# Kernel optimization log

Measured on AMD Instinct MI355X. Metric: run time of the kernel, lower is better.

## Reference

```python
import jax, jax.numpy as jnp
import numpy as np

N_MAX_L = (24, 20, 16, 12)   # basis size per angular channel l
N_SPECIES = 4
HIDDEN = 32
N_PAIRS = 1_500_000


def setup_inputs() -> dict:
    key = jax.random.key(0)
    ks = jax.random.split(key, 2 + 4 * len(N_MAX_L))
    inp = {
        "radial_functions": jax.random.normal(ks[0], (N_PAIRS, sum(N_MAX_L)), jnp.float32),
        "neighbor_species": jax.random.randint(ks[1], (N_PAIRS,), 0, N_SPECIES),
    }
    i = 2
    for l, n in enumerate(N_MAX_L):
        inp[f"w1_l{l}"] = jax.random.normal(ks[i], (N_SPECIES, n, HIDDEN), jnp.float32) * (n ** -0.5); i += 1
        inp[f"w2_l{l}"] = jax.random.normal(ks[i], (N_SPECIES, HIDDEN, HIDDEN), jnp.float32) * (HIDDEN ** -0.5); i += 1
        inp[f"w3_l{l}"] = jax.random.normal(ks[i], (N_SPECIES, HIDDEN, HIDDEN), jnp.float32) * (HIDDEN ** -0.5); i += 1
        inp[f"w4_l{l}"] = jax.random.normal(ks[i], (N_SPECIES, HIDDEN, n), jnp.float32) * (HIDDEN ** -0.5); i += 1
    return inp


def _species_mlp(x, neighbor_species, w1, w2, w3, w4):
    # x: [N, n_l]; weights: [S, ...]. For each row, apply the MLP of its species.
    # Equivalent to the torch gather -> tiny MLP -> scatter per species.
    out = jnp.zeros_like(x)
    for s in range(N_SPECIES):
        h = jax.nn.silu(x @ w1[s])
        h = jax.nn.silu(h @ w2[s])
        h = jax.nn.silu(h @ w3[s])
        y = h @ w4[s]
        out = jnp.where((neighbor_species == s)[:, None], y, out)
    return out


def reference(radial_functions, neighbor_species,
              w1_l0, w2_l0, w3_l0, w4_l0,
              w1_l1, w2_l1, w3_l1, w4_l1,
              w1_l2, w2_l2, w3_l2, w4_l2,
              w1_l3, w2_l3, w3_l3, w4_l3):
    ws = [(w1_l0, w2_l0, w3_l0, w4_l0),
          (w1_l1, w2_l1, w3_l1, w4_l1),
          (w1_l2, w2_l2, w3_l2, w4_l2),
          (w1_l3, w2_l3, w3_l3, w4_l3)]
    outs = []
    idx = 0
    for l, n in enumerate(N_MAX_L):
        x = radial_functions[:, idx:idx + n]
        idx += n
        outs.append(_species_mlp(x, neighbor_species, *ws[l]))
    # torch version returns a list of per-l blocks; we return them concatenated
    # along the feature axis ([N, sum(n_max_l)]) for a single-array output.
    return jnp.concatenate(outs, axis=1)
```

## Files before the change

kernel.cpp:

```cpp
#include <hip/hip_runtime.h>

typedef __attribute__((ext_vector_type(8))) short bf16x8;
typedef __attribute__((ext_vector_type(16))) float f32x16;

union FragU { bf16x8 v; unsigned int u[4]; };
struct Wptrs { const float* p[16]; };

#define ROWS 256
#define THREADS 512

__device__ __forceinline__ unsigned int bfb(float f) {
  unsigned int u = __builtin_bit_cast(unsigned int, f);
  return (u + 0x7fffu + ((u >> 16) & 1u)) >> 16;
}
__device__ __forceinline__ unsigned int cvtpk(float lo, float hi) {
  unsigned int d;
  asm("v_cvt_pk_bf16_f32 %0, %1, %2" : "=v"(d) : "v"(lo), "v"(hi));
  return d;
}
__device__ __forceinline__ float bf2f(unsigned short b) {
  return __builtin_bit_cast(float, (unsigned int)b << 16);
}
__device__ __forceinline__ float silu_f(float x) {
  float e = __builtin_amdgcn_exp2f(-1.4426950408889634f * x);
  return x * __builtin_amdgcn_rcpf(1.0f + e);
}
__device__ __forceinline__ f32x16 zero16() {
  f32x16 z;
  #pragma unroll
  for (int i = 0; i < 16; ++i) z[i] = 0.0f;
  return z;
}
__device__ __forceinline__ bf16x8 ldA(const unsigned short* __restrict__ wsb, int tile, int l31, int hi, int h) {
  return *(const bf16x8*)(wsb + ((tile * 32 + l31) << 5) + h * 16 + hi * 8);
}

__device__ __forceinline__ void transition(const f32x16& acc, bf16x8& b0, bf16x8& b1) {
  unsigned int P[8];
  #pragma unroll
  for (int t = 0; t < 8; ++t)
    P[t] = cvtpk(silu_f(acc[2*t]), silu_f(acc[2*t+1]));
  asm volatile("v_permlane32_swap_b32 %0, %1" : "+v"(P[0]), "+v"(P[2]));
  asm volatile("v_permlane32_swap_b32 %0, %1" : "+v"(P[1]), "+v"(P[3]));
  asm volatile("v_permlane32_swap_b32 %0, %1" : "+v"(P[4]), "+v"(P[6]));
  asm volatile("v_permlane32_swap_b32 %0, %1" : "+v"(P[5]), "+v"(P[7]));
  FragU f0, f1;
  f0.u[0] = P[0]; f0.u[1] = P[1]; f0.u[2] = P[2]; f0.u[3] = P[3];
  f1.u[0] = P[4]; f1.u[1] = P[5]; f1.u[2] = P[6]; f1.u[3] = P[7];
  b0 = f0.v; b1 = f1.v;
}

template<int NL, int OFF, int TB, int SI>
__device__ __forceinline__ void phase(const float* __restrict__ rad,
    const unsigned short* __restrict__ wsb,
    unsigned short* s_in, unsigned short* s_out, const unsigned short* s_pos,
    const int* s_cnt, const int* s_off, const int* s_gpre,
    int base, int vb, int tid)
{
  constexpr int QPR = NL / 4;
  __syncthreads();
  {
    int4 z = make_int4(0, 0, 0, 0);
    #pragma unroll
    for (int i = 0; i < (ROWS * 32) / (8 * THREADS); ++i)
      ((int4*)s_in)[i * THREADS + tid] = z;
  }
  __syncthreads();
  for (int j = tid; j < vb * QPR; j += THREADS) {
    int i = j / QPR, q = j - i * QPR;
    float4 g = *(const float4*)(rad + (long)(base + i) * 72 + OFF + q * 4);
    int dst = s_pos[i];
    *(uint2*)(s_in + dst * SI + q * 4) = make_uint2(cvtpk(g.x, g.y), cvtpk(g.z, g.w));
  }
  __syncthreads();

  const int lane = tid & 63, wid = tid >> 6;
  const int l31 = lane & 31, hi = lane >> 5;
  const int Gtot = s_gpre[4];
  for (int g = wid; g < Gtot; g += THREADS / 64) {
    int s = (g >= s_gpre[1]) + (g >= s_gpre[2]) + (g >= s_gpre[3]);
    int gi = g - s_gpre[s];
    int goff = s_off[s] + gi * 32;
    int gcnt = s_cnt[s] - gi * 32; if (gcnt > 32) gcnt = 32;
    int li = l31 < gcnt ? l31 : gcnt - 1;
    int row = goff + li;

    FragU bx0, bx1;
    bx0.v = *(const bf16x8*)(s_in + row * SI + hi * 8);
    if (NL > 16) bx1.v = *(const bf16x8*)(s_in + row * SI + 16 + hi * 8);

    f32x16 acc = zero16();
    acc = __builtin_amdgcn_mfma_f32_32x32x16_bf16(ldA(wsb, TB + s, l31, hi, 0), bx0.v, acc, 0, 0, 0);
    if (NL > 16)
      acc = __builtin_amdgcn_mfma_f32_32x32x16_bf16(ldA(wsb, TB + s, l31, hi, 1), bx1.v, acc, 0, 0, 0);
    bf16x8 b0, b1;
    transition(acc, b0, b1);
    acc = zero16();
    acc = __builtin_amdgcn_mfma_f32_32x32x16_bf16(ldA(wsb, TB + 4 + s, l31, hi, 0), b0, acc, 0, 0, 0);
    acc = __builtin_amdgcn_mfma_f32_32x32x16_bf16(ldA(wsb, TB + 4 + s, l31, hi, 1), b1, acc, 0, 0, 0);
    transition(acc, b0, b1);
    acc = zero16();
    acc = __builtin_amdgcn_mfma_f32_32x32x16_bf16(ldA(wsb, TB + 8 + s, l31, hi, 0), b0, acc, 0, 0, 0);
    acc = __builtin_amdgcn_mfma_f32_32x32x16_bf16(ldA(wsb, TB + 8 + s, l31, hi, 1), b1, acc, 0, 0, 0);
    transition(acc, b0, b1);
    acc = zero16();
    acc = __builtin_amdgcn_mfma_f32_32x32x16_bf16(ldA(wsb, TB + 12 + s, l31, hi, 0), b0, acc, 0, 0, 0);
    acc = __builtin_amdgcn_mfma_f32_32x32x16_bf16(ldA(wsb, TB + 12 + s, l31, hi, 1), b1, acc, 0, 0, 0);

    if (l31 < gcnt) {
      int obase = (goff + l31) * 72 + OFF;
      #pragma unroll
      for (int t = 0; t < 4; ++t) {
        if (8 * t + 4 * hi + 4 <= NL) {
          *(uint2*)(s_out + obase + 8 * t + 4 * hi) =
              make_uint2(cvtpk(acc[4*t], acc[4*t+1]), cvtpk(acc[4*t+2], acc[4*t+3]));
        }
      }
    }
  }
}

__global__ void convert_weights_kernel(Wptrs wp, unsigned short* __restrict__ wsb) {
  int idx = blockIdx.x * 256 + threadIdx.x;
  const int NLs[4] = {24, 20, 16, 12};
  int l = idx >> 14, r = idx & 16383;
  int tile = r >> 10, j = (r >> 5) & 31, k = r & 31;
  int s = tile & 3, layer = tile >> 2;
  int NL = NLs[l];
  const float* w = wp.p[l * 4 + layer];
  float v = 0.0f;
  if (layer == 0)      { if (k < NL) v = w[(s * NL + k) * 32 + j]; }
  else if (layer == 3) { if (j < NL) v = w[(s * 32 + k) * NL + j]; }
  else                 { v = w[(s * 32 + k) * 32 + j]; }
  wsb[idx] = (unsigned short)bfb(v);
}

__global__ __launch_bounds__(THREADS, 6) void RadialBasis_51316269253437_kernel(
    const float* __restrict__ rad, const int* __restrict__ spc,
    const unsigned short* __restrict__ wsb, float* __restrict__ out, int npairs)
{
  __shared__ unsigned short s_in[ROWS * 32];
  __shared__ unsigned short s_out[ROWS * 72];
  __shared__ unsigned short s_pos[ROWS];
  __shared__ int s_cnt[4], s_fill[4], s_off[4], s_gpre[5];
  const int tid = threadIdx.x;
  const int base = blockIdx.x * ROWS;
  int vb = npairs - base; if (vb > ROWS) vb = ROWS;

  if (tid < 4) { s_cnt[tid] = 0; s_fill[tid] = 0; }
  __syncthreads();
  int sp = -1;
  if (tid < vb) sp = spc[base + tid];
  if (sp >= 0) atomicAdd(&s_cnt[sp], 1);
  __syncthreads();
  if (tid == 0) {
    int o = 0, gp = 0;
    #pragma unroll
    for (int s4 = 0; s4 < 4; ++s4) {
      s_off[s4] = o; o += s_cnt[s4];
      s_gpre[s4] = gp; gp += (s_cnt[s4] + 31) >> 5;
    }
    s_gpre[4] = gp;
  }
  __syncthreads();
  if (sp >= 0) {
    int pos = s_off[sp] + atomicAdd(&s_fill[sp], 1);
    s_pos[tid] = (unsigned short)pos;
  }
  phase<24,  0,  0, 32>(rad, wsb, s_in, s_out, s_pos, s_cnt, s_off, s_gpre, base, vb, tid);
  phase<20, 24, 16, 32>(rad, wsb, s_in, s_out, s_pos, s_cnt, s_off, s_gpre, base, vb, tid);
  phase<16, 44, 32, 24>(rad, wsb, s_in, s_out, s_pos, s_cnt, s_off, s_gpre, base, vb, tid);
  phase<12, 60, 48, 24>(rad, wsb, s_in, s_out, s_pos, s_cnt, s_off, s_gpre, base, vb, tid);
  __syncthreads();

  for (int j = tid; j < vb * 18; j += THREADS) {
    int i = j / 18, q = j - i * 18;
    uint2 w = *(const uint2*)(s_out + (int)s_pos[i] * 72 + q * 4);
    float4 v = make_float4(bf2f((unsigned short)(w.x & 0xffff)),
                           bf2f((unsigned short)(w.x >> 16)),
                           bf2f((unsigned short)(w.y & 0xffff)),
                           bf2f((unsigned short)(w.y >> 16)));
    *(float4*)(out + (long)(base + i) * 72 + q * 4) = v;
  }
}

extern "C" void kernel_launch(void* const* d_in, const int* in_sizes, int n_in,
                              void* d_out, int out_size, void* d_ws, size_t ws_size,
                              hipStream_t stream) {
  const float* rad = (const float*)d_in[0];
  const int* spc = (const int*)d_in[1];
  Wptrs wp;
  for (int i = 0; i < 16; ++i) wp.p[i] = (const float*)d_in[2 + i];
  float* out = (float*)d_out;
  unsigned short* wsb = (unsigned short*)d_ws;
  int npairs = in_sizes[0] / 72;

  convert_weights_kernel<<<dim3(256), dim3(256), 0, stream>>>(wp, wsb);
  int grid = (npairs + ROWS - 1) / ROWS;
  RadialBasis_51316269253437_kernel<<<dim3(grid), dim3(THREADS), 0, stream>>>(rad, spc, wsb, out, npairs);
}
```

Baseline: 361.8 us.

## Write MLP outputs directly to global memory and drop shared output staging

Removes the shared-memory output buffer and its final bf16-to-fp32 copy-out loop. Each phase now writes fp32 results straight to global memory through an inverse permutation array. The separate zero-fill pass is folded into the input staging loop, which writes zeros for unused columns. Rows per block double to 512 and the launch-bounds occupancy hint rises to 8. The cost is scattered 16-byte global stores per row instead of coalesced row-order stores.

```diff
diff --git a/kernel.cpp b/kernel.cpp
--- a/kernel.cpp
+++ b/kernel.cpp
@@ -6,7 +6,7 @@
 union FragU { bf16x8 v; unsigned int u[4]; };
 struct Wptrs { const float* p[16]; };
 
-#define ROWS 256
+#define ROWS 512
 #define THREADS 512
 
 __device__ __forceinline__ unsigned int bfb(float f) {
@@ -17,9 +17,6 @@
   unsigned int d;
   asm("v_cvt_pk_bf16_f32 %0, %1, %2" : "=v"(d) : "v"(lo), "v"(hi));
   return d;
-}
-__device__ __forceinline__ float bf2f(unsigned short b) {
-  return __builtin_bit_cast(float, (unsigned int)b << 16);
 }
 __device__ __forceinline__ float silu_f(float x) {
   float e = __builtin_amdgcn_exp2f(-1.4426950408889634f * x);
@@ -50,27 +47,23 @@
   b0 = f0.v; b1 = f1.v;
 }
 
-template<int NL, int OFF, int TB, int SI>
+template<int NL, int OFF, int TB>
 __device__ __forceinline__ void phase(const float* __restrict__ rad,
-    const unsigned short* __restrict__ wsb,
-    unsigned short* s_in, unsigned short* s_out, const unsigned short* s_pos,
+    float* __restrict__ out, const unsigned short* __restrict__ wsb,
+    unsigned short* s_in, const unsigned short* s_pos, const unsigned short* s_perm,
     const int* s_cnt, const int* s_off, const int* s_gpre,
     int base, int vb, int tid)
 {
   constexpr int QPR = NL / 4;
   __syncthreads();
-  {
-    int4 z = make_int4(0, 0, 0, 0);
-    #pragma unroll
-    for (int i = 0; i < (ROWS * 32) / (8 * THREADS); ++i)
-      ((int4*)s_in)[i * THREADS + tid] = z;
-  }
-  __syncthreads();
-  for (int j = tid; j < vb * QPR; j += THREADS) {
-    int i = j / QPR, q = j - i * QPR;
-    float4 g = *(const float4*)(rad + (long)(base + i) * 72 + OFF + q * 4);
-    int dst = s_pos[i];
-    *(uint2*)(s_in + dst * SI + q * 4) = make_uint2(cvtpk(g.x, g.y), cvtpk(g.z, g.w));
+  for (int j = tid; j < vb * 8; j += THREADS) {
+    int i = j >> 3, q = j & 7;
+    uint2 w = make_uint2(0u, 0u);
+    if (q < QPR) {
+      float4 g = *(const float4*)(rad + (long)(base + i) * 72 + OFF + q * 4);
+      w = make_uint2(cvtpk(g.x, g.y), cvtpk(g.z, g.w));
+    }
+    *(uint2*)(s_in + (int)s_pos[i] * 32 + q * 4) = w;
   }
   __syncthreads();
 
@@ -86,8 +79,8 @@
     int row = goff + li;
 
     FragU bx0, bx1;
-    bx0.v = *(const bf16x8*)(s_in + row * SI + hi * 8);
-    if (NL > 16) bx1.v = *(const bf16x8*)(s_in + row * SI + 16 + hi * 8);
+    bx0.v = *(const bf16x8*)(s_in + row * 32 + hi * 8);
+    if (NL > 16) bx1.v = *(const bf16x8*)(s_in + row * 32 + 16 + hi * 8);
 
     f32x16 acc = zero16();
     acc = __builtin_amdgcn_mfma_f32_32x32x16_bf16(ldA(wsb, TB + s, l31, hi, 0), bx0.v, acc, 0, 0, 0);
@@ -108,12 +101,12 @@
     acc = __builtin_amdgcn_mfma_f32_32x32x16_bf16(ldA(wsb, TB + 12 + s, l31, hi, 1), b1, acc, 0, 0, 0);
 
     if (l31 < gcnt) {
-      int obase = (goff + l31) * 72 + OFF;
+      float* op = out + (long)(base + (int)s_perm[goff + l31]) * 72 + OFF;
       #pragma unroll
       for (int t = 0; t < 4; ++t) {
         if (8 * t + 4 * hi + 4 <= NL) {
-          *(uint2*)(s_out + obase + 8 * t + 4 * hi) =
-              make_uint2(cvtpk(acc[4*t], acc[4*t+1]), cvtpk(acc[4*t+2], acc[4*t+3]));
+          *(float4*)(op + 8 * t + 4 * hi) =
+              make_float4(acc[4*t], acc[4*t+1], acc[4*t+2], acc[4*t+3]);
         }
       }
     }
@@ -135,13 +128,13 @@
   wsb[idx] = (unsigned short)bfb(v);
 }
 
-__global__ __launch_bounds__(THREADS, 6) void RadialBasis_51316269253437_kernel(
+__global__ __launch_bounds__(THREADS, 8) void RadialBasis_51316269253437_kernel(
     const float* __restrict__ rad, const int* __restrict__ spc,
     const unsigned short* __restrict__ wsb, float* __restrict__ out, int npairs)
 {
   __shared__ unsigned short s_in[ROWS * 32];
-  __shared__ unsigned short s_out[ROWS * 72];
   __shared__ unsigned short s_pos[ROWS];
+  __shared__ unsigned short s_perm[ROWS];
   __shared__ int s_cnt[4], s_fill[4], s_off[4], s_gpre[5];
   const int tid = threadIdx.x;
   const int base = blockIdx.x * ROWS;
@@ -166,22 +159,12 @@
   if (sp >= 0) {
     int pos = s_off[sp] + atomicAdd(&s_fill[sp], 1);
     s_pos[tid] = (unsigned short)pos;
+    s_perm[pos] = (unsigned short)tid;
   }
-  phase<24,  0,  0, 32>(rad, wsb, s_in, s_out, s_pos, s_cnt, s_off, s_gpre, base, vb, tid);
-  phase<20, 24, 16, 32>(rad, wsb, s_in, s_out, s_pos, s_cnt, s_off, s_gpre, base, vb, tid);
-  phase<16, 44, 32, 24>(rad, wsb, s_in, s_out, s_pos, s_cnt, s_off, s_gpre, base, vb, tid);
-  phase<12, 60, 48, 24>(rad, wsb, s_in, s_out, s_pos, s_cnt, s_off, s_gpre, base, vb, tid);
-  __syncthreads();
-
-  for (int j = tid; j < vb * 18; j += THREADS) {
-    int i = j / 18, q = j - i * 18;
-    uint2 w = *(const uint2*)(s_out + (int)s_pos[i] * 72 + q * 4);
-    float4 v = make_float4(bf2f((unsigned short)(w.x & 0xffff)),
-                           bf2f((unsigned short)(w.x >> 16)),
-                           bf2f((unsigned short)(w.y & 0xffff)),
-                           bf2f((unsigned short)(w.y >> 16)));
-    *(float4*)(out + (long)(base + i) * 72 + q * 4) = v;
-  }
+  phase<24,  0,  0>(rad, out, wsb, s_in, s_pos, s_perm, s_cnt, s_off, s_gpre, base, vb, tid);
+  phase<20, 24, 16>(rad, out, wsb, s_in, s_pos, s_perm, s_cnt, s_off, s_gpre, base, vb, tid);
+  phase<16, 44, 32>(rad, out, wsb, s_in, s_pos, s_perm, s_cnt, s_off, s_gpre, base, vb, tid);
+  phase<12, 60, 48>(rad, out, wsb, s_in, s_pos, s_perm, s_cnt, s_off, s_gpre, base, vb, tid);
 }
 
 extern "C" void kernel_launch(void* const* d_in, const int* in_sizes, int n_in,
```

Result: slower. 455.2 us (+25.8%).
